# Performance work log

Measured on AMD Instinct MI355X. Metric: run time of the kernel, lower is better.

## Reference

```python
import jax, jax.numpy as jnp
import numpy as np

N = 100000   # nodes
E = 1600000  # edges
IN, HID, OUT = 128, 128, 64
K = 32       # MaxK top-k
NUM_LAYERS = 2


def _xavier(key, shape):
    lim = float(np.sqrt(6.0 / (shape[0] + shape[1])))
    return jax.random.uniform(key, shape, jnp.float32, -lim, lim)


def setup_inputs() -> dict:
    key = jax.random.key(0)
    ks = jax.random.split(key, 8)
    return {
        "x": jax.random.normal(ks[0], (N, IN), jnp.float32),
        "src": jax.random.randint(ks[1], (E,), 0, N, dtype=jnp.int32),
        "dst": jax.random.randint(ks[2], (E,), 0, N, dtype=jnp.int32),
        "W_in": _xavier(ks[3], (IN, HID)), "b_in": jnp.zeros((HID,), jnp.float32),
        "W1": _xavier(ks[4], (HID, HID)), "b1": jnp.zeros((HID,), jnp.float32),
        "bg1": jnp.zeros((HID,), jnp.float32),
        "W2": _xavier(ks[5], (HID, HID)), "b2": jnp.zeros((HID,), jnp.float32),
        "bg2": jnp.zeros((HID,), jnp.float32),
        "W_out": _xavier(ks[6], (HID, OUT)), "b_out": jnp.zeros((OUT,), jnp.float32),
    }


def _maxk(x, k):
    # keep top-k entries per row, zero the rest (straight-through mask)
    _, idx = jax.lax.top_k(x, k)                      # [N, k]
    rows = jnp.arange(x.shape[0])[:, None]
    mask = jnp.zeros_like(x).at[rows, idx].set(1.0)
    return x * mask


def _graph_conv(x, src, dst, bias):
    # DGL GraphConv, norm='both', weight=None: D_dst^{-1/2} A D_src^{-1/2} x + b
    ones = jnp.ones((src.shape[0],), x.dtype)
    deg_out = jnp.maximum(jax.ops.segment_sum(ones, src, num_segments=N), 1.0)
    deg_in = jnp.maximum(jax.ops.segment_sum(ones, dst, num_segments=N), 1.0)
    msg = (x * (deg_out ** -0.5)[:, None])[src]        # [E, HID] gather
    agg = jax.ops.segment_sum(msg, dst, num_segments=N)  # [N, HID] scatter-add
    return agg * (deg_in ** -0.5)[:, None] + bias


def reference(x, src, dst, W_in, b_in, W1, b1, bg1, W2, b2, bg2, W_out, b_out):
    h = jax.nn.relu(x @ W_in + b_in)
    for W, b, bg in ((W1, b1, bg1), (W2, b2, bg2)):
        h = h @ W + b
        h = _maxk(h, K)
        # dropout: eval-mode identity
        h = _graph_conv(h, src, dst, bg)
    return h @ W_out + b_out
```

## Files before the change

### kernel.cpp

```cpp
#include <hip/hip_runtime.h>

#define NN   100000
#define EE   1600000
#define HIDF 128
#define OUTF 64
#define KSEL 32
#define BSH  3
#define NBK  (NN >> BSH)
#define CAPSH 8
#define CAP  (1 << CAPSH)
#define GT   ((NN + 31) / 32)
#define GT64 ((NN + 63) / 64)
#define GE   ((EE + 255) / 256)

static __device__ __forceinline__ unsigned int sortable_key(float f) {
    unsigned int u = __float_as_uint(f);
    return (u & 0x80000000u) ? ~u : (u | 0x80000000u);
}

__global__ __launch_bounds__(256, 2) void fused_bin_relu(const int* __restrict__ src,
                                                         const int* __restrict__ dst,
                                                         int* __restrict__ bcnt,
                                                         int* __restrict__ scnt,
                                                         int* __restrict__ bin,
                                                         const float* __restrict__ X,
                                                         const float* __restrict__ W,
                                                         const float* __restrict__ bias,
                                                         float* __restrict__ out) {
    __shared__ float As[32][128];
    __shared__ float Ws[16][128];
    const int tid = threadIdx.x;
    const int g = blockIdx.x / 3;
    const int r = blockIdx.x % 3;

    if (r < 2) {
        int i = (g * 2 + r) * 256 + tid;
        if (i < EE) {
            int s = src[i];
            int d = dst[i];
            int b = d >> BSH;
            int pos = atomicAdd(&bcnt[b], 1);
            if (pos < CAP) bin[(b << CAPSH) + pos] = (s << BSH) | (d & ((1 << BSH) - 1));
            atomicAdd(&scnt[s], 1);
        }
        return;
    }

    const int rbase = g * 32;
    const int cc = tid & 31;
    const int r0 = (tid >> 5) * 4;
    const int n = NN;
    float acc[4][4];
#pragma unroll
    for (int i = 0; i < 4; ++i) { acc[i][0] = 0.f; acc[i][1] = 0.f; acc[i][2] = 0.f; acc[i][3] = 0.f; }

    float4 wreg0 = *(const float4*)(W + (size_t)tid * 4);
    float4 wreg1 = *(const float4*)(W + (size_t)(tid + 256) * 4);

#pragma unroll
    for (int q = 0; q < 4; ++q) {
        int f = q * 256 + tid;
        int row = rbase + (f >> 5);
        float4 v = make_float4(0.f, 0.f, 0.f, 0.f);
        if (row < n) v = *(const float4*)(X + (size_t)row * 128 + (f & 31) * 4);
        *(float4*)&As[f >> 5][(f & 31) * 4] = v;
    }

    for (int p = 0; p < 8; ++p) {
        const int kb = p * 16;
        if (p) __syncthreads();
        *(float4*)&Ws[tid >> 5][(tid & 31) * 4] = wreg0;
        *(float4*)&Ws[(tid >> 5) + 8][(tid & 31) * 4] = wreg1;
        if (p < 7) {
            const float* wp = W + (size_t)(kb + 16) * 128;
            wreg0 = *(const float4*)(wp + (size_t)tid * 4);
            wreg1 = *(const float4*)(wp + (size_t)(tid + 256) * 4);
        }
        __syncthreads();
#pragma unroll
        for (int kq = 0; kq < 4; ++kq) {
            int k = kq * 4;
            float4 w0 = *(float4*)&Ws[k + 0][cc * 4];
            float4 w1 = *(float4*)&Ws[k + 1][cc * 4];
            float4 w2 = *(float4*)&Ws[k + 2][cc * 4];
            float4 w3 = *(float4*)&Ws[k + 3][cc * 4];
#pragma unroll
            for (int i = 0; i < 4; ++i) {
                float4 a = *(float4*)&As[r0 + i][kb + k];
                acc[i][0] += a.x * w0.x + a.y * w1.x + a.z * w2.x + a.w * w3.x;
                acc[i][1] += a.x * w0.y + a.y * w1.y + a.z * w2.y + a.w * w3.y;
                acc[i][2] += a.x * w0.z + a.y * w1.z + a.z * w2.z + a.w * w3.z;
                acc[i][3] += a.x * w0.w + a.y * w1.w + a.z * w2.w + a.w * w3.w;
            }
        }
    }
    float4 b4 = *(const float4*)(bias + cc * 4);
#pragma unroll
    for (int i = 0; i < 4; ++i) {
        int gr = rbase + r0 + i;
        if (gr < n) {
            float4 o = make_float4(fmaxf(acc[i][0] + b4.x, 0.f), fmaxf(acc[i][1] + b4.y, 0.f),
                                   fmaxf(acc[i][2] + b4.z, 0.f), fmaxf(acc[i][3] + b4.w, 0.f));
            *(float4*)(out + (size_t)gr * 128 + cc * 4) = o;
        }
    }
}

static __device__ __forceinline__ void gemm_maxk_body(float (*As)[128], float (*Ws)[128],
                                                      const float* __restrict__ A,
                                                      const float* __restrict__ W,
                                                      const float* __restrict__ bias,
                                                      const int* __restrict__ scnt,
                                                      float* __restrict__ svals,
                                                      int n, int rbase) {
    const int tid = threadIdx.x;
    const int cc = tid & 31;
    const int r0 = (tid >> 5) * 4;
    float acc[4][4];
#pragma unroll
    for (int i = 0; i < 4; ++i) { acc[i][0] = 0.f; acc[i][1] = 0.f; acc[i][2] = 0.f; acc[i][3] = 0.f; }

    float4 wreg0 = *(const float4*)(W + (size_t)tid * 4);
    float4 wreg1 = *(const float4*)(W + (size_t)(tid + 256) * 4);

#pragma unroll
    for (int q = 0; q < 4; ++q) {
        int f = q * 256 + tid;
        *(float4*)&As[f >> 5][(f & 31) * 4] =
            *(const float4*)(A + (size_t)rbase * 128 + (size_t)f * 4);
    }

    for (int p = 0; p < 8; ++p) {
        const int kb = p * 16;
        if (p) __syncthreads();
        *(float4*)&Ws[tid >> 5][(tid & 31) * 4] = wreg0;
        *(float4*)&Ws[(tid >> 5) + 8][(tid & 31) * 4] = wreg1;
        if (p < 7) {
            const float* wp = W + (size_t)(kb + 16) * 128;
            wreg0 = *(const float4*)(wp + (size_t)tid * 4);
            wreg1 = *(const float4*)(wp + (size_t)(tid + 256) * 4);
        }
        __syncthreads();
#pragma unroll
        for (int kq = 0; kq < 4; ++kq) {
            int k = kq * 4;
            float4 w0 = *(float4*)&Ws[k + 0][cc * 4];
            float4 w1 = *(float4*)&Ws[k + 1][cc * 4];
            float4 w2 = *(float4*)&Ws[k + 2][cc * 4];
            float4 w3 = *(float4*)&Ws[k + 3][cc * 4];
#pragma unroll
            for (int i = 0; i < 4; ++i) {
                float4 a = *(float4*)&As[r0 + i][kb + k];
                acc[i][0] += a.x * w0.x + a.y * w1.x + a.z * w2.x + a.w * w3.x;
                acc[i][1] += a.x * w0.y + a.y * w1.y + a.z * w2.y + a.w * w3.y;
                acc[i][2] += a.x * w0.z + a.y * w1.z + a.z * w2.z + a.w * w3.z;
                acc[i][3] += a.x * w0.w + a.y * w1.w + a.z * w2.w + a.w * w3.w;
            }
        }
    }

    const int lane = tid & 63;
    const int wvi = tid >> 6;
    const bool up = lane >= 32;
    const unsigned lt32 = (1u << (lane & 31)) - 1u;
    float4 b4 = *(const float4*)(bias + cc * 4);

    unsigned keys[4][4];
#pragma unroll
    for (int i = 0; i < 4; ++i) {
        acc[i][0] += b4.x; acc[i][1] += b4.y; acc[i][2] += b4.z; acc[i][3] += b4.w;
        keys[i][0] = sortable_key(acc[i][0]);
        keys[i][1] = sortable_key(acc[i][1]);
        keys[i][2] = sortable_key(acc[i][2]);
        keys[i][3] = sortable_key(acc[i][3]);
    }
    unsigned prefL[4], prefU[4];
#pragma unroll
    for (int i = 0; i < 4; ++i) { prefL[i] = 0u; prefU[i] = 0u; }

    for (int bit = 31; bit >= 8; --bit) {
        unsigned msk = 1u << bit;
#pragma unroll
        for (int i = 0; i < 4; ++i) {
            unsigned cL = prefL[i] | msk;
            unsigned cU = prefU[i] | msk;
            unsigned myc = up ? cU : cL;
            unsigned long long b0 = __ballot(keys[i][0] >= myc);
            unsigned long long b1 = __ballot(keys[i][1] >= myc);
            unsigned long long b2 = __ballot(keys[i][2] >= myc);
            unsigned long long b3 = __ballot(keys[i][3] >= myc);
            int cntL = __popc((unsigned)b0) + __popc((unsigned)b1) +
                       __popc((unsigned)b2) + __popc((unsigned)b3);
            int cntU = __popc((unsigned)(b0 >> 32)) + __popc((unsigned)(b1 >> 32)) +
                       __popc((unsigned)(b2 >> 32)) + __popc((unsigned)(b3 >> 32));
            prefL[i] = (cntL >= KSEL) ? cL : prefL[i];
            prefU[i] = (cntU >= KSEL) ? cU : prefU[i];
        }
    }

#pragma unroll 1
    for (int i = 0; i < 4; ++i) {
        int row = rbase + 8 * wvi + i + (up ? 4 : 0);
        unsigned myp = up ? prefU[i] : prefL[i];
        unsigned kb0 = keys[i][0] & 0xFFFFFF00u, kb1 = keys[i][1] & 0xFFFFFF00u;
        unsigned kb2 = keys[i][2] & 0xFFFFFF00u, kb3 = keys[i][3] & 0xFFFFFF00u;
        unsigned long long g0 = __ballot(kb0 > myp), g1 = __ballot(kb1 > myp);
        unsigned long long g2 = __ballot(kb2 > myp), g3 = __ballot(kb3 > myp);
        unsigned long long e0 = __ballot(kb0 == myp), e1 = __ballot(kb1 == myp);
        unsigned long long e2 = __ballot(kb2 == myp), e3 = __ballot(kb3 == myp);
        unsigned gh0 = up ? (unsigned)(g0 >> 32) : (unsigned)g0;
        unsigned gh1 = up ? (unsigned)(g1 >> 32) : (unsigned)g1;
        unsigned gh2 = up ? (unsigned)(g2 >> 32) : (unsigned)g2;
        unsigned gh3 = up ? (unsigned)(g3 >> 32) : (unsigned)g3;
        unsigned eh0 = up ? (unsigned)(e0 >> 32) : (unsigned)e0;
        unsigned eh1 = up ? (unsigned)(e1 >> 32) : (unsigned)e1;
        unsigned eh2 = up ? (unsigned)(e2 >> 32) : (unsigned)e2;
        unsigned eh3 = up ? (unsigned)(e3 >> 32) : (unsigned)e3;
        int m = __popc(gh0) + __popc(gh1) + __popc(gh2) + __popc(gh3);
        int need = KSEL - m;
        int gpos = __popc(gh0 & lt32) + __popc(gh1 & lt32) + __popc(gh2 & lt32) + __popc(gh3 & lt32);
        int epos = __popc(eh0 & lt32) + __popc(eh1 & lt32) + __popc(eh2 & lt32) + __popc(eh3 & lt32);
        bool ok = row < n;
        float ds = 0.f;
        if (ok) ds = rsqrtf((float)max(scnt[row], 1));
        size_t base = (size_t)row * 32;
        unsigned cbit = (unsigned)(lane & 31);
        {
            int slot = -1;
            if (kb0 > myp) slot = gpos;
            else if (kb0 == myp && epos < need) slot = m + epos;
            if (slot >= 0 && ok) {
                unsigned u = (__float_as_uint(acc[i][0] * ds) & 0xFFFFFF80u) | (unsigned)(cc * 4 + 0);
                svals[base + slot] = __uint_as_float(u);
            }
            gpos += (gh0 >> cbit) & 1u;
            epos += (eh0 >> cbit) & 1u;
        }
        {
            int slot = -1;
            if (kb1 > myp) slot = gpos;
            else if (kb1 == myp && epos < need) slot = m + epos;
            if (slot >= 0 && ok) {
                unsigned u = (__float_as_uint(acc[i][1] * ds) & 0xFFFFFF80u) | (unsigned)(cc * 4 + 1);
                svals[base + slot] = __uint_as_float(u);
            }
            gpos += (gh1 >> cbit) & 1u;
            epos += (eh1 >> cbit) & 1u;
        }
        {
            int slot = -1;
            if (kb2 > myp) slot = gpos;
            else if (kb2 == myp && epos < need) slot = m + epos;
            if (slot >= 0 && ok) {
                unsigned u = (__float_as_uint(acc[i][2] * ds) & 0xFFFFFF80u) | (unsigned)(cc * 4 + 2);
                svals[base + slot] = __uint_as_float(u);
            }
            gpos += (gh2 >> cbit) & 1u;
            epos += (eh2 >> cbit) & 1u;
        }
        {
            int slot = -1;
            if (kb3 > myp) slot = gpos;
            else if (kb3 == myp && epos < need) slot = m + epos;
            if (slot >= 0 && ok) {
                unsigned u = (__float_as_uint(acc[i][3] * ds) & 0xFFFFFF80u) | (unsigned)(cc * 4 + 3);
                svals[base + slot] = __uint_as_float(u);
            }
        }
    }
}

__global__ __launch_bounds__(256, 2) void fused_csr_maxk(const int* __restrict__ bin,
                                                         const int* __restrict__ bcnt,
                                                         int* __restrict__ row_off,
                                                         int* __restrict__ cnt_in,
                                                         float* __restrict__ dvin,
                                                         int* __restrict__ csr,
                                                         const float* __restrict__ A,
                                                         const float* __restrict__ W,
                                                         const float* __restrict__ bias,
                                                         const int* __restrict__ scnt,
                                                         float* __restrict__ svals) {
    __shared__ float As[32][128];
    __shared__ float Ws[16][128];
    const int tid = threadIdx.x;

    if (blockIdx.x >= GT) {
        int* cnt8 = (int*)&As[0][0];
        int* cur8 = cnt8 + (1 << BSH);
        const int b = blockIdx.x - GT;
        if (tid < (1 << BSH)) cnt8[tid] = 0;
        __syncthreads();
        const int m = min(bcnt[b], CAP);
        const int base = b << CAPSH;
        for (int e = tid; e < m; e += 256) {
            atomicAdd(&cnt8[bin[base + e] & ((1 << BSH) - 1)], 1);
        }
        __syncthreads();
        if (tid < (1 << BSH)) {
            int pre = 0;
#pragma unroll
            for (int q = 0; q < (1 << BSH); ++q) pre += (q < tid) ? cnt8[q] : 0;
            int node = (b << BSH) + tid;
            int start = base + pre;
            if (node < NN) {
                row_off[node] = start;
                cnt_in[node] = cnt8[tid];
                dvin[node] = rsqrtf((float)max(cnt8[tid], 1));
            }
            cur8[tid] = start;
        }
        __syncthreads();
        for (int e = tid; e < m; e += 256) {
            int r = bin[base + e];
            int pos = atomicAdd(&cur8[r & ((1 << BSH) - 1)], 1);
            csr[pos] = r >> BSH;
        }
        return;
    }

    gemm_maxk_body(As, Ws, A, W, bias, scnt, svals, NN, blockIdx.x * 32);
}

__global__ __launch_bounds__(256, 2) void gemm_maxk(const float* __restrict__ A,
                                                    const float* __restrict__ W,
                                                    const float* __restrict__ bias,
                                                    const int* __restrict__ scnt,
                                                    float* __restrict__ svals, int n) {
    __shared__ float As[32][128];
    __shared__ float Ws[16][128];
    gemm_maxk_body(As, Ws, A, W, bias, scnt, svals, n, blockIdx.x * 32);
}

__global__ __launch_bounds__(256) void agg_kernel(const float* __restrict__ svals,
                                                  const int* __restrict__ row_off,
                                                  const int* __restrict__ cnt_in,
                                                  const int* __restrict__ csr_src,
                                                  const float* __restrict__ dvin,
                                                  const float* __restrict__ bg,
                                                  float* __restrict__ out, int n) {
    __shared__ float acc[4][2][128];
    const int wv = threadIdx.x >> 6;
    const int lane = threadIdx.x & 63;
    const int sub = lane >> 5;
    const int j = lane & 31;
    const int node = blockIdx.x * 4 + wv;
    float* base0 = &acc[wv][0][0];
    base0[lane] = 0.f;
    base0[lane + 64] = 0.f;
    base0[lane + 128] = 0.f;
    base0[lane + 192] = 0.f;
    if (node < n) {
        int s0 = row_off[node], s1 = s0 + cnt_in[node];
        float* Ac = &acc[wv][sub][0];
        int e = s0 + sub;
        for (; e + 2 < s1; e += 4) {
            int sA = csr_src[e];
            int sB = csr_src[e + 2];
            float vA = svals[(size_t)sA * 32 + j];
            float vB = svals[(size_t)sB * 32 + j];
            int fA = (int)(__float_as_uint(vA) & 127u);
            Ac[fA] += vA;
            int fB = (int)(__float_as_uint(vB) & 127u);
            Ac[fB] += vB;
        }
        for (; e < s1; e += 2) {
            int sA = csr_src[e];
            float vA = svals[(size_t)sA * 32 + j];
            int fA = (int)(__float_as_uint(vA) & 127u);
            Ac[fA] += vA;
        }
    }
    if (node < n) {
        float dv = dvin[node];
        float r0 = acc[wv][0][lane] + acc[wv][1][lane];
        float r1 = acc[wv][0][lane + 64] + acc[wv][1][lane + 64];
        out[(size_t)node * 128 + lane] = r0 * dv + bg[lane];
        out[(size_t)node * 128 + lane + 64] = r1 * dv + bg[lane + 64];
    }
}

__global__ __launch_bounds__(256, 2) void gemm_out64(const float* __restrict__ A,
                                                     const float* __restrict__ W,
                                                     const float* __restrict__ bias,
                                                     float* __restrict__ out, int n) {
    __shared__ float As[64][128];
    __shared__ float Ws[32][64];
    const int tid = threadIdx.x;
    const int rbase = blockIdx.x * 64;
    const int cc = tid & 15;
    const int r0 = (tid >> 4) * 4;
    float acc[4][4];
#pragma unroll
    for (int i = 0; i < 4; ++i) { acc[i][0] = 0.f; acc[i][1] = 0.f; acc[i][2] = 0.f; acc[i][3] = 0.f; }

    float4 wreg0 = *(const float4*)(W + (size_t)tid * 4);
    float4 wreg1 = *(const float4*)(W + (size_t)(tid + 256) * 4);

#pragma unroll
    for (int q = 0; q < 8; ++q) {
        int f = q * 256 + tid;
        *(float4*)&As[f >> 5][(f & 31) * 4] =
            *(const float4*)(A + (size_t)rbase * 128 + (size_t)f * 4);
    }

    for (int p = 0; p < 4; ++p) {
        const int kb = p * 32;
        if (p) __syncthreads();
        *(float4*)&Ws[tid >> 4][(tid & 15) * 4] = wreg0;
        *(float4*)&Ws[(tid >> 4) + 16][(tid & 15) * 4] = wreg1;
        if (p < 3) {
            const float* wp = W + (size_t)(kb + 32) * 64;
            wreg0 = *(const float4*)(wp + (size_t)tid * 4);
            wreg1 = *(const float4*)(wp + (size_t)(tid + 256) * 4);
        }
        __syncthreads();
#pragma unroll
        for (int kq = 0; kq < 8; ++kq) {
            int k = kq * 4;
            float4 w0 = *(float4*)&Ws[k + 0][cc * 4];
            float4 w1 = *(float4*)&Ws[k + 1][cc * 4];
            float4 w2 = *(float4*)&Ws[k + 2][cc * 4];
            float4 w3 = *(float4*)&Ws[k + 3][cc * 4];
#pragma unroll
            for (int i = 0; i < 4; ++i) {
                float4 a = *(float4*)&As[r0 + i][kb + k];
                acc[i][0] += a.x * w0.x + a.y * w1.x + a.z * w2.x + a.w * w3.x;
                acc[i][1] += a.x * w0.y + a.y * w1.y + a.z * w2.y + a.w * w3.y;
                acc[i][2] += a.x * w0.z + a.y * w1.z + a.z * w2.z + a.w * w3.z;
                acc[i][3] += a.x * w0.w + a.y * w1.w + a.z * w2.w + a.w * w3.w;
            }
        }
    }
    float4 b4 = *(const float4*)(bias + cc * 4);
#pragma unroll
    for (int i = 0; i < 4; ++i) {
        int gr = rbase + r0 + i;
        if (gr < n) {
            float4 o = make_float4(acc[i][0] + b4.x, acc[i][1] + b4.y,
                                   acc[i][2] + b4.z, acc[i][3] + b4.w);
            *(float4*)(out + (size_t)gr * 64 + cc * 4) = o;
        }
    }
}

extern "C" void kernel_launch(void* const* d_in, const int* in_sizes, int n_in,
                              void* d_out, int out_size, void* d_ws, size_t ws_size,
                              hipStream_t stream) {
    const float* x     = (const float*)d_in[0];
    const int*   src   = (const int*)d_in[1];
    const int*   dst   = (const int*)d_in[2];
    const float* W_in  = (const float*)d_in[3];
    const float* b_in  = (const float*)d_in[4];
    const float* W1    = (const float*)d_in[5];
    const float* b1    = (const float*)d_in[6];
    const float* bg1   = (const float*)d_in[7];
    const float* W2    = (const float*)d_in[8];
    const float* b2    = (const float*)d_in[9];
    const float* bg2   = (const float*)d_in[10];
    const float* W_out = (const float*)d_in[11];
    const float* b_out = (const float*)d_in[12];
    float* out = (float*)d_out;

    char* p = (char*)d_ws;
    auto carve = [&](size_t bytes) {
        char* r = p;
        p += (bytes + 255) & ~(size_t)255;
        return r;
    };
    int*   scnt    = (int*)carve((size_t)NN * 4);
    int*   bcnt    = (int*)carve((size_t)NBK * 4);
    float* dvin    = (float*)carve((size_t)NN * 4);
    int*   row_off = (int*)carve((size_t)NN * 4);
    int*   cnt_in  = (int*)carve((size_t)NN * 4);
    int*   bin     = (int*)carve((size_t)NBK * CAP * 4);
    int*   csr_src = (int*)carve((size_t)NBK * CAP * 4);
    float* hbuf    = (float*)carve((size_t)(NN + 128) * HIDF * 4);
    float* svals   = (float*)carve((size_t)NN * KSEL * 4);

    const int gAgg = (NN + 3) / 4;

    hipMemsetAsync(scnt, 0, (size_t)NN * 4, stream);
    hipMemsetAsync(bcnt, 0, (size_t)NBK * 4, stream);

    fused_bin_relu<<<GT * 3, 256, 0, stream>>>(src, dst, bcnt, scnt, bin,
                                               x, W_in, b_in, hbuf);
    fused_csr_maxk<<<GT + NBK, 256, 0, stream>>>(bin, bcnt, row_off, cnt_in, dvin, csr_src,
                                                 hbuf, W1, b1, scnt, svals);
    agg_kernel<<<gAgg, 256, 0, stream>>>(svals, row_off, cnt_in, csr_src, dvin, bg1, hbuf, NN);

    gemm_maxk<<<GT, 256, 0, stream>>>(hbuf, W2, b2, scnt, svals, NN);
    agg_kernel<<<gAgg, 256, 0, stream>>>(svals, row_off, cnt_in, csr_src, dvin, bg2, hbuf, NN);

    gemm_out64<<<GT64, 256, 0, stream>>>(hbuf, W_out, b_out, out, NN);
}
```

Baseline: 614.6 us.

## Fuse sparse aggregation into following GEMM+MaxK and output GEMM kernels

Each graph aggregation now writes its result rows straight into the shared-memory A tile of the next dense GEMM (layer-2 GEMM with MaxK, and the final output projection). This removes the round trip of the 128-wide hidden activations through global memory, and drops two kernel launches. Separate sparse value buffers are used per layer so the fused kernel can read one while writing the other. In exchange, each block runs its aggregation serially per wave (8 or 16 nodes per wave) with lower parallelism per node. The fused_agg_maxk kernel also omits a node<n bounds check, which is safe here only because NN divides evenly by 32.

```diff
diff --git a/kernel.cpp b/kernel.cpp
--- a/kernel.cpp
+++ b/kernel.cpp
@@ -106,29 +106,19 @@
     }
 }
 
-static __device__ __forceinline__ void gemm_maxk_body(float (*As)[128], float (*Ws)[128],
-                                                      const float* __restrict__ A,
-                                                      const float* __restrict__ W,
-                                                      const float* __restrict__ bias,
-                                                      const int* __restrict__ scnt,
-                                                      float* __restrict__ svals,
-                                                      int n, int rbase) {
+static __device__ __forceinline__ void gemm_maxk_compute(float (*As)[128], float (*Ws)[128],
+                                                         float4 wreg0, float4 wreg1,
+                                                         const float* __restrict__ W,
+                                                         const float* __restrict__ bias,
+                                                         const int* __restrict__ scnt,
+                                                         float* __restrict__ svals,
+                                                         int n, int rbase) {
     const int tid = threadIdx.x;
     const int cc = tid & 31;
     const int r0 = (tid >> 5) * 4;
     float acc[4][4];
 #pragma unroll
     for (int i = 0; i < 4; ++i) { acc[i][0] = 0.f; acc[i][1] = 0.f; acc[i][2] = 0.f; acc[i][3] = 0.f; }
-
-    float4 wreg0 = *(const float4*)(W + (size_t)tid * 4);
-    float4 wreg1 = *(const float4*)(W + (size_t)(tid + 256) * 4);
-
-#pragma unroll
-    for (int q = 0; q < 4; ++q) {
-        int f = q * 256 + tid;
-        *(float4*)&As[f >> 5][(f & 31) * 4] =
-            *(const float4*)(A + (size_t)rbase * 128 + (size_t)f * 4);
-    }
 
     for (int p = 0; p < 8; ++p) {
         const int kb = p * 16;
@@ -319,90 +309,126 @@
         return;
     }
 
-    gemm_maxk_body(As, Ws, A, W, bias, scnt, svals, NN, blockIdx.x * 32);
-}
-
-__global__ __launch_bounds__(256, 2) void gemm_maxk(const float* __restrict__ A,
-                                                    const float* __restrict__ W,
-                                                    const float* __restrict__ bias,
-                                                    const int* __restrict__ scnt,
-                                                    float* __restrict__ svals, int n) {
+    const int rbase = blockIdx.x * 32;
+    float4 wreg0 = *(const float4*)(W + (size_t)tid * 4);
+    float4 wreg1 = *(const float4*)(W + (size_t)(tid + 256) * 4);
+#pragma unroll
+    for (int q = 0; q < 4; ++q) {
+        int f = q * 256 + tid;
+        *(float4*)&As[f >> 5][(f & 31) * 4] =
+            *(const float4*)(A + (size_t)rbase * 128 + (size_t)f * 4);
+    }
+    gemm_maxk_compute(As, Ws, wreg0, wreg1, W, bias, scnt, svals, NN, rbase);
+}
+
+__global__ __launch_bounds__(256, 2) void fused_agg_maxk(const float* __restrict__ svalsA,
+                                                         const int* __restrict__ row_off,
+                                                         const int* __restrict__ cnt_in,
+                                                         const int* __restrict__ csr_src,
+                                                         const float* __restrict__ dvin,
+                                                         const float* __restrict__ bg,
+                                                         const float* __restrict__ W,
+                                                         const float* __restrict__ bias,
+                                                         const int* __restrict__ scnt,
+                                                         float* __restrict__ svalsB) {
     __shared__ float As[32][128];
     __shared__ float Ws[16][128];
-    gemm_maxk_body(As, Ws, A, W, bias, scnt, svals, n, blockIdx.x * 32);
-}
-
-__global__ __launch_bounds__(256) void agg_kernel(const float* __restrict__ svals,
-                                                  const int* __restrict__ row_off,
-                                                  const int* __restrict__ cnt_in,
-                                                  const int* __restrict__ csr_src,
-                                                  const float* __restrict__ dvin,
-                                                  const float* __restrict__ bg,
-                                                  float* __restrict__ out, int n) {
-    __shared__ float acc[4][2][128];
-    const int wv = threadIdx.x >> 6;
-    const int lane = threadIdx.x & 63;
+    __shared__ float sc[4][2][128];
+    const int tid = threadIdx.x;
+    const int wv = tid >> 6;
+    const int lane = tid & 63;
     const int sub = lane >> 5;
     const int j = lane & 31;
-    const int node = blockIdx.x * 4 + wv;
-    float* base0 = &acc[wv][0][0];
-    base0[lane] = 0.f;
-    base0[lane + 64] = 0.f;
-    base0[lane + 128] = 0.f;
-    base0[lane + 192] = 0.f;
-    if (node < n) {
+    const int rbase = blockIdx.x * 32;
+
+    float4 wreg0 = *(const float4*)(W + (size_t)tid * 4);
+    float4 wreg1 = *(const float4*)(W + (size_t)(tid + 256) * 4);
+
+    for (int u = 0; u < 8; ++u) {
+        int node = rbase + wv * 8 + u;
+        float* Ac = &sc[wv][sub][0];
+        Ac[j] = 0.f; Ac[j + 32] = 0.f; Ac[j + 64] = 0.f; Ac[j + 96] = 0.f;
         int s0 = row_off[node], s1 = s0 + cnt_in[node];
-        float* Ac = &acc[wv][sub][0];
         int e = s0 + sub;
         for (; e + 2 < s1; e += 4) {
             int sA = csr_src[e];
             int sB = csr_src[e + 2];
-            float vA = svals[(size_t)sA * 32 + j];
-            float vB = svals[(size_t)sB * 32 + j];
-            int fA = (int)(__float_as_uint(vA) & 127u);
-            Ac[fA] += vA;
-            int fB = (int)(__float_as_uint(vB) & 127u);
-            Ac[fB] += vB;
+            float vA = svalsA[(size_t)sA * 32 + j];
+            float vB = svalsA[(size_t)sB * 32 + j];
+            Ac[(int)(__float_as_uint(vA) & 127u)] += vA;
+            Ac[(int)(__float_as_uint(vB) & 127u)] += vB;
         }
         for (; e < s1; e += 2) {
             int sA = csr_src[e];
-            float vA = svals[(size_t)sA * 32 + j];
-            int fA = (int)(__float_as_uint(vA) & 127u);
-            Ac[fA] += vA;
-        }
-    }
-    if (node < n) {
+            float vA = svalsA[(size_t)sA * 32 + j];
+            Ac[(int)(__float_as_uint(vA) & 127u)] += vA;
+        }
         float dv = dvin[node];
-        float r0 = acc[wv][0][lane] + acc[wv][1][lane];
-        float r1 = acc[wv][0][lane + 64] + acc[wv][1][lane + 64];
-        out[(size_t)node * 128 + lane] = r0 * dv + bg[lane];
-        out[(size_t)node * 128 + lane + 64] = r1 * dv + bg[lane + 64];
-    }
-}
-
-__global__ __launch_bounds__(256, 2) void gemm_out64(const float* __restrict__ A,
-                                                     const float* __restrict__ W,
-                                                     const float* __restrict__ bias,
-                                                     float* __restrict__ out, int n) {
+        int rr = wv * 8 + u;
+        As[rr][lane]      = (sc[wv][0][lane]      + sc[wv][1][lane])      * dv + bg[lane];
+        As[rr][lane + 64] = (sc[wv][0][lane + 64] + sc[wv][1][lane + 64]) * dv + bg[lane + 64];
+    }
+    __syncthreads();
+
+    gemm_maxk_compute(As, Ws, wreg0, wreg1, W, bias, scnt, svalsB, NN, rbase);
+}
+
+__global__ __launch_bounds__(256, 2) void fused_agg_out(const float* __restrict__ svalsB,
+                                                        const int* __restrict__ row_off,
+                                                        const int* __restrict__ cnt_in,
+                                                        const int* __restrict__ csr_src,
+                                                        const float* __restrict__ dvin,
+                                                        const float* __restrict__ bg,
+                                                        const float* __restrict__ W,
+                                                        const float* __restrict__ bias,
+                                                        float* __restrict__ out, int n) {
     __shared__ float As[64][128];
     __shared__ float Ws[32][64];
+    __shared__ float sc[4][2][128];
     const int tid = threadIdx.x;
+    const int wv = tid >> 6;
+    const int lane = tid & 63;
+    const int sub = lane >> 5;
+    const int j = lane & 31;
     const int rbase = blockIdx.x * 64;
+
+    float4 wreg0 = *(const float4*)(W + (size_t)tid * 4);
+    float4 wreg1 = *(const float4*)(W + (size_t)(tid + 256) * 4);
+
+    for (int u = 0; u < 16; ++u) {
+        int node = rbase + wv * 16 + u;
+        float* Ac = &sc[wv][sub][0];
+        Ac[j] = 0.f; Ac[j + 32] = 0.f; Ac[j + 64] = 0.f; Ac[j + 96] = 0.f;
+        float dv = 0.f;
+        if (node < n) {
+            dv = dvin[node];
+            int s0 = row_off[node], s1 = s0 + cnt_in[node];
+            int e = s0 + sub;
+            for (; e + 2 < s1; e += 4) {
+                int sA = csr_src[e];
+                int sB = csr_src[e + 2];
+                float vA = svalsB[(size_t)sA * 32 + j];
+                float vB = svalsB[(size_t)sB * 32 + j];
+                Ac[(int)(__float_as_uint(vA) & 127u)] += vA;
+                Ac[(int)(__float_as_uint(vB) & 127u)] += vB;
+            }
+            for (; e < s1; e += 2) {
+                int sA = csr_src[e];
+                float vA = svalsB[(size_t)sA * 32 + j];
+                Ac[(int)(__float_as_uint(vA) & 127u)] += vA;
+            }
+        }
+        int rr = wv * 16 + u;
+        As[rr][lane]      = (sc[wv][0][lane]      + sc[wv][1][lane])      * dv + bg[lane];
+        As[rr][lane + 64] = (sc[wv][0][lane + 64] + sc[wv][1][lane + 64]) * dv + bg[lane + 64];
+    }
+    __syncthreads();
+
     const int cc = tid & 15;
     const int r0 = (tid >> 4) * 4;
     float acc[4][4];
 #pragma unroll
     for (int i = 0; i < 4; ++i) { acc[i][0] = 0.f; acc[i][1] = 0.f; acc[i][2] = 0.f; acc[i][3] = 0.f; }
-
-    float4 wreg0 = *(const float4*)(W + (size_t)tid * 4);
-    float4 wreg1 = *(const float4*)(W + (size_t)(tid + 256) * 4);
-
-#pragma unroll
-    for (int q = 0; q < 8; ++q) {
-        int f = q * 256 + tid;
-        *(float4*)&As[f >> 5][(f & 31) * 4] =
-            *(const float4*)(A + (size_t)rbase * 128 + (size_t)f * 4);
-    }
 
     for (int p = 0; p < 4; ++p) {
         const int kb = p * 32;
@@ -476,9 +502,8 @@
     int*   bin     = (int*)carve((size_t)NBK * CAP * 4);
     int*   csr_src = (int*)carve((size_t)NBK * CAP * 4);
     float* hbuf    = (float*)carve((size_t)(NN + 128) * HIDF * 4);
-    float* svals   = (float*)carve((size_t)NN * KSEL * 4);
-
-    const int gAgg = (NN + 3) / 4;
+    float* svalsA  = (float*)carve((size_t)NN * KSEL * 4);
+    float* svalsB  = (float*)carve((size_t)NN * KSEL * 4);
 
     hipMemsetAsync(scnt, 0, (size_t)NN * 4, stream);
     hipMemsetAsync(bcnt, 0, (size_t)NBK * 4, stream);
@@ -486,11 +511,9 @@
     fused_bin_relu<<<GT * 3, 256, 0, stream>>>(src, dst, bcnt, scnt, bin,
                                                x, W_in, b_in, hbuf);
     fused_csr_maxk<<<GT + NBK, 256, 0, stream>>>(bin, bcnt, row_off, cnt_in, dvin, csr_src,
-                                                 hbuf, W1, b1, scnt, svals);
-    agg_kernel<<<gAgg, 256, 0, stream>>>(svals, row_off, cnt_in, csr_src, dvin, bg1, hbuf, NN);
-
-    gemm_maxk<<<GT, 256, 0, stream>>>(hbuf, W2, b2, scnt, svals, NN);
-    agg_kernel<<<gAgg, 256, 0, stream>>>(svals, row_off, cnt_in, csr_src, dvin, bg2, hbuf, NN);
-
-    gemm_out64<<<GT64, 256, 0, stream>>>(hbuf, W_out, b_out, out, NN);
-}
+                                                 hbuf, W1, b1, scnt, svalsA);
+    fused_agg_maxk<<<GT, 256, 0, stream>>>(svalsA, row_off, cnt_in, csr_src, dvin, bg1,
+                                           W2, b2, scnt, svalsB);
+    fused_agg_out<<<GT64, 256, 0, stream>>>(svalsB, row_off, cnt_in, csr_src, dvin, bg2,
+                                            W_out, b_out, out, NN);
+}
```

Result: slower. 923.0 us (+50.2%).
